# Kernel tuning notes

Hardware: AMD Instinct MI355X
Metric: run time of the kernel (lower is better)

Reference implementation:

```python
import jax, jax.numpy as jnp
import numpy as np

EPS = 1e-5

def _layernorm(x, g, b):
    # LayerNorm over last dim (head_dim), eps=1e-5 like nn.LayerNorm
    mu = jnp.mean(x, axis=-1, keepdims=True)
    var = jnp.mean(jnp.square(x - mu), axis=-1, keepdims=True)
    return (x - mu) * jax.lax.rsqrt(var + EPS) * g + b

def _rotate_half(x):
    d = x.shape[-1] // 2
    return jnp.concatenate([-x[..., d:], x[..., :d]], axis=-1)

def _apply_rotary(x, cos, sin):
    # x: [B,S,H,D]; cos/sin: [S,D] broadcast over batch and heads
    c = cos[None, :, None, :]
    s = sin[None, :, None, :]
    return x * c + _rotate_half(x) * s

def setup_inputs() -> dict:
    key = jax.random.key(0)
    ks = jax.random.split(key, 16)
    B, S, Dm = 2, 1024, 2048
    H, Hkv, Dh = 16, 4, 128
    f = lambda k, shp: (jax.random.normal(k, shp, dtype=jnp.float32) * 0.02)
    return {
        "hidden_states": jax.random.normal(ks[0], (B, S, Dm), dtype=jnp.float32),
        "cos": jax.random.uniform(ks[1], (S, Dh), dtype=jnp.float32),
        "sin": jax.random.uniform(ks[2], (S, Dh), dtype=jnp.float32),
        "Wq": f(ks[3], (H * Dh, Dm)),   "bq": jnp.zeros((H * Dh,), jnp.float32),
        "Wk": f(ks[4], (Hkv * Dh, Dm)), "bk": jnp.zeros((Hkv * Dh,), jnp.float32),
        "Wv": f(ks[5], (Hkv * Dh, Dm)), "bv": jnp.zeros((Hkv * Dh,), jnp.float32),
        "Wo": f(ks[6], (Dm, H * Dh)),   "bo": jnp.zeros((Dm,), jnp.float32),
        "qn_g": jnp.ones((Dh,), jnp.float32), "qn_b": jnp.zeros((Dh,), jnp.float32),
        "kn_g": jnp.ones((Dh,), jnp.float32), "kn_b": jnp.zeros((Dh,), jnp.float32),
        "cu_seqlens": jnp.array([0, S, 2 * S], dtype=jnp.int32),
        "max_s": 1024,
    }

def reference(hidden_states, cos, sin, Wq, bq, Wk, bk, Wv, bv, Wo, bo,
              qn_g, qn_b, kn_g, kn_b, cu_seqlens, max_s):
    B, S, Dm = hidden_states.shape
    Dh = qn_g.shape[0]
    H = Wq.shape[0] // Dh
    Hkv = Wk.shape[0] // Dh
    scale = 1.0 / jnp.sqrt(jnp.float32(Dh))

    q = (hidden_states @ Wq.T + bq).reshape(B, S, H, Dh)
    k = (hidden_states @ Wk.T + bk).reshape(B, S, Hkv, Dh)
    v = (hidden_states @ Wv.T + bv).reshape(B, S, Hkv, Dh)

    q = _apply_rotary(_layernorm(q, qn_g, qn_b), cos, sin)
    k = _apply_rotary(_layernorm(k, kn_g, kn_b), cos, sin)

    # GQA: repeat_interleave kv heads to match q heads
    n_rep = H // Hkv
    if n_rep > 1:
        k = jnp.repeat(k, n_rep, axis=2)
        v = jnp.repeat(v, n_rep, axis=2)

    # scores: [B,H,S,S]
    scores = jnp.einsum('bqhd,bkhd->bhqk', q, k) * scale
    causal = jnp.tril(jnp.ones((S, S), dtype=bool))
    scores = jnp.where(causal[None, None], scores, jnp.finfo(scores.dtype).min)
    weights = jax.nn.softmax(scores, axis=-1)
    out = jnp.einsum('bhqk,bkhd->bqhd', weights, v).reshape(B, S, H * Dh)
    return out @ Wo.T + bo
```

## Files before the change

kernel.cpp:

```cpp
#include <hip/hip_runtime.h>
#include <cmath>

typedef __attribute__((ext_vector_type(8))) short bf16x8;
typedef __attribute__((ext_vector_type(4))) short s16x4;
typedef __attribute__((ext_vector_type(4))) float f32x4;

#define MFMA_BF16 __builtin_amdgcn_mfma_f32_16x16x32_bf16

__device__ __forceinline__ float bf2f(short s) {
    unsigned u = ((unsigned)(unsigned short)s) << 16;
    return __builtin_bit_cast(float, u);
}
__device__ __forceinline__ short f2bf(float f) {
    unsigned u = __builtin_bit_cast(unsigned, f);
    u += 0x7fffu + ((u >> 16) & 1u);
    return (short)(u >> 16);
}

__device__ __forceinline__ void gl_lds16(const short* gp, short* lp) {
    __builtin_amdgcn_global_load_lds(
        (const __attribute__((address_space(1))) unsigned int*)gp,
        (__attribute__((address_space(3))) unsigned int*)lp, 16, 0, 0);
}

__global__ __launch_bounds__(256) void cvt5(
    const float* s0, short* d0, int n0,
    const float* s1, short* d1, int n1,
    const float* s2, short* d2, int n2,
    const float* s3, short* d3, int n3,
    const float* s4, short* d4, int n4)
{
    long long i = (long long)blockIdx.x * 1024 + threadIdx.x * 4;
    const float* s; short* d;
    if      (i < n0)                  { s = s0; d = d0; }
    else if ((i -= n0) < n1)          { s = s1; d = d1; }
    else if ((i -= n1) < n2)          { s = s2; d = d2; }
    else if ((i -= n2) < n3)          { s = s3; d = d3; }
    else      { i -= n3;                s = s4; d = d4; }
    float4 v = *(const float4*)(s + i);
    s16x4 o;
    o[0] = f2bf(v.x); o[1] = f2bf(v.y); o[2] = f2bf(v.z); o[3] = f2bf(v.w);
    *(s16x4*)(d + i) = o;
}

template <int MODE>
__global__ __launch_bounds__(256) void gemm_t(
    const short* __restrict__ A, const short* __restrict__ W,
    const float* __restrict__ bq, const float* __restrict__ bk,
    const float* __restrict__ bv,
    short* __restrict__ qo, short* __restrict__ ko, short* __restrict__ vo,
    float* __restrict__ fo,
    int M, int K, int S, int Hkv, int Nq, int Nkv, int N)
{
    __shared__ __align__(16) short As[2][2 * 8 * 512];
    __shared__ __align__(16) short Bs[2][2 * 4 * 512];

    const int w    = threadIdx.x >> 6;
    const int lane = threadIdx.x & 63;
    const int l15  = lane & 15;
    const int quad = lane >> 4;
    const int wy   = w >> 1;
    const int wx   = w & 1;
    const int m0   = blockIdx.y * 128;
    const int n0   = blockIdx.x * 64;

    const short* Ab = A + (size_t)m0 * K;
    const short* Wb = W + (size_t)n0 * K;

    const int srow = lane >> 2;
    const int scol = ((lane & 3) ^ ((srow >> 1) & 3)) * 8;
    auto stage = [&](int buf, int kofs) {
#pragma unroll
        for (int h2 = 0; h2 < 2; h2++) {
#pragma unroll
            for (int i = 0; i < 2; i++) {
                const int c = 2 * w + i;
                gl_lds16(Ab + (size_t)(c * 16 + srow) * K + kofs + h2 * 32 + scol,
                         As[buf] + h2 * 4096 + c * 512 + lane * 8);
            }
            gl_lds16(Wb + (size_t)(w * 16 + srow) * K + kofs + h2 * 32 + scol,
                     Bs[buf] + h2 * 2048 + w * 512 + lane * 8);
        }
    };

    f32x4 acc[4][2];
#pragma unroll
    for (int i = 0; i < 4; i++)
#pragma unroll
        for (int j = 0; j < 2; j++) acc[i][j] = f32x4{0.f, 0.f, 0.f, 0.f};

    const int ridx = (l15 * 4 + (quad ^ ((l15 >> 1) & 3))) * 8;
    const int nk = K / 64;
    stage(0, 0);
    __syncthreads();

    for (int kt = 0; kt < nk; kt++) {
        const int cur = kt & 1;
        if (kt + 1 < nk) stage(cur ^ 1, (kt + 1) * 64);

#pragma unroll
        for (int h2 = 0; h2 < 2; h2++) {
            bf16x8 af[4], bfr[2];
#pragma unroll
            for (int i = 0; i < 4; i++)
                af[i] = *(const bf16x8*)(As[cur] + h2 * 4096 + (wy * 4 + i) * 512 + ridx);
#pragma unroll
            for (int j = 0; j < 2; j++)
                bfr[j] = *(const bf16x8*)(Bs[cur] + h2 * 2048 + (wx * 2 + j) * 512 + ridx);
#pragma unroll
            for (int i = 0; i < 4; i++)
#pragma unroll
                for (int j = 0; j < 2; j++)
                    acc[i][j] = MFMA_BF16(af[i], bfr[j], acc[i][j], 0, 0, 0);
        }
        __syncthreads();
    }

#pragma unroll
    for (int i = 0; i < 4; i++) {
#pragma unroll
        for (int j = 0; j < 2; j++) {
            const int col = n0 + wx * 32 + j * 16 + l15;
#pragma unroll
            for (int r = 0; r < 4; r++) {
                const int row = m0 + wy * 64 + i * 16 + quad * 4 + r;
                float v = acc[i][j][r];
                if constexpr (MODE == 0) {
                    if (col < Nq) {
                        qo[(size_t)row * Nq + col] = f2bf(v + bq[col]);
                    } else if (col < Nq + Nkv) {
                        int cn = col - Nq;
                        ko[(size_t)row * Nkv + cn] = f2bf(v + bk[cn]);
                    } else {
                        int cn = col - Nq - Nkv;
                        int b  = row / S, s = row - b * S;
                        int hk = cn >> 7, dh = cn & 127;
                        vo[(size_t)((b * Hkv + hk) * 128 + dh) * S + s] = f2bf(v + bv[cn]);
                    }
                } else {
                    fo[(size_t)row * N + col] = v + bq[col];
                }
            }
        }
    }
}

__global__ __launch_bounds__(256) void ln_rope2(
    const short* __restrict__ Xq, short* __restrict__ Yq,
    const short* __restrict__ Xk, short* __restrict__ Yk,
    const float* __restrict__ qg, const float* __restrict__ qbe,
    const float* __restrict__ kg, const float* __restrict__ kbe,
    const float* __restrict__ cosp, const float* __restrict__ sinp,
    int H, int Hkv, int S, int nq)
{
    int gw = blockIdx.x * 4 + (threadIdx.x >> 6);
    const int lane = threadIdx.x & 63;
    const short* X; short* Y; const float* g; const float* bt; int Hc;
    if (gw < nq) { X = Xq; Y = Yq; g = qg; bt = qbe; Hc = H; }
    else { gw -= nq; X = Xk; Y = Yk; g = kg; bt = kbe; Hc = Hkv; }

    const int h  = gw % Hc;
    const int rs = gw / Hc;
    const int b  = rs / S;
    const int s  = rs - b * S;

    const short* x = X + ((size_t)rs * Hc + h) * 128;
    float x0 = bf2f(x[lane]), x1 = bf2f(x[lane + 64]);

    float sum = x0 + x1;
    float sq  = x0 * x0 + x1 * x1;
#pragma unroll
    for (int off = 32; off > 0; off >>= 1) {
        sum += __shfl_xor(sum, off, 64);
        sq  += __shfl_xor(sq, off, 64);
    }
    float mu  = sum * (1.f / 128.f);
    float var = sq * (1.f / 128.f) - mu * mu;
    float rinv = rsqrtf(var + 1e-5f);

    float y0 = (x0 - mu) * rinv * g[lane]      + bt[lane];
    float y1 = (x1 - mu) * rinv * g[lane + 64] + bt[lane + 64];

    float c0 = cosp[(size_t)s * 128 + lane];
    float c1 = cosp[(size_t)s * 128 + lane + 64];
    float s0 = sinp[(size_t)s * 128 + lane];
    float s1 = sinp[(size_t)s * 128 + lane + 64];

    float o0 = y0 * c0 - y1 * s0;
    float o1 = y1 * c1 + y0 * s1;

    short* yp = Y + ((size_t)(b * Hc + h) * S + s) * 128;
    yp[lane]      = f2bf(o0);
    yp[lane + 64] = f2bf(o1);
}

__global__ __launch_bounds__(256, 2) void attn(
    const short* __restrict__ Q, const short* __restrict__ Kt,
    const short* __restrict__ Vt, short* __restrict__ O,
    int S, int H, int Hkv, int nrep, float scale)
{
    __shared__ __align__(16) short Ks[2][16 * 512];
    __shared__ __align__(16) short Vs[2][16 * 512];
    __shared__ __align__(16) short P[4][16][72];

    const int w    = threadIdx.x >> 6;
    const int lane = threadIdx.x & 63;
    const int l15  = lane & 15;
    const int quad = lane >> 4;
    const int bh   = blockIdx.x;
    const int h    = bh % H;
    const int b    = bh / H;
    const int nyt  = gridDim.y;
    const int y    = blockIdx.y;
    const int qblk = (y < (nyt >> 1)) ? (nyt - 1 - y) : (y - (nyt >> 1));
    const int hk   = h / nrep;
    const int m0   = qblk * 64 + w * 16;
    const int qpos = m0 + l15;

    const short* qb = Q  + (size_t)(b * H + h) * S * 128;
    const short* kb = Kt + (size_t)(b * Hkv + hk) * S * 128;
    const short* vb = Vt + (size_t)(b * Hkv + hk) * 128 * S;

    auto stage = [&](int buf, int j0) {
#pragma unroll
        for (int i = 0; i < 8; i++) {
            if (w < 2) {
                const int s = w * 8 + i;
                const int t = s >> 2, c = s & 3;
                gl_lds16(kb + (size_t)(j0 + t * 16 + l15) * 128 + c * 32 + quad * 8,
                         Ks[buf] + s * 512 + lane * 8);
            } else {
                const int u = (w - 2) * 8 + i;
                const int c = u >> 1, hf = u & 1;
                gl_lds16(vb + (size_t)(c * 16 + l15) * S + j0 + hf * 32 + quad * 8,
                         Vs[buf] + u * 512 + lane * 8);
            }
        }
    };

    bf16x8 qf[4];
#pragma unroll
    for (int c = 0; c < 4; c++)
        qf[c] = *(const bf16x8*)(qb + (size_t)(m0 + l15) * 128 + c * 32 + quad * 8);

    f32x4 of[8];
#pragma unroll
    for (int c = 0; c < 8; c++) of[c] = f32x4{0.f, 0.f, 0.f, 0.f};
    float m_s = -1e30f, l_s = 0.f;
    const float c2 = scale * 1.44269504f;

    const int nkt = qblk + 1;
    stage(0, 0);
    __syncthreads();

    for (int kt = 0; kt < nkt; kt++) {
        const int cur = kt & 1;
        if (kt + 1 < nkt) stage(cur ^ 1, (kt + 1) * 64);

        const short* Kb = Ks[cur];
        const short* Vb = Vs[cur];
        const int j0 = kt * 64;

        f32x4 sc[4];
#pragma unroll
        for (int t = 0; t < 4; t++) sc[t] = f32x4{0.f, 0.f, 0.f, 0.f};
#pragma unroll
        for (int c = 0; c < 4; c++)
#pragma unroll
            for (int t = 0; t < 4; t++) {
                bf16x8 kf = *(const bf16x8*)(Kb + (t * 4 + c) * 512 + lane * 8);
                sc[t] = MFMA_BF16(kf, qf[c], sc[t], 0, 0, 0);
            }

        float v[4][4];
        float mx = -1e30f;
#pragma unroll
        for (int t = 0; t < 4; t++)
#pragma unroll
            for (int r = 0; r < 4; r++) {
                float s_ = sc[t][r];
                if (j0 + t * 16 + quad * 4 + r > qpos) s_ = -1e30f;
                v[t][r] = s_;
                mx = fmaxf(mx, s_);
            }
        mx = fmaxf(mx, __shfl_xor(mx, 16, 64));
        mx = fmaxf(mx, __shfl_xor(mx, 32, 64));
        float mnew  = fmaxf(m_s, mx);
        float mc    = mnew * c2;
        float alpha = exp2f(m_s * c2 - mc);
        float sum = 0.f;
        float p[4][4];
#pragma unroll
        for (int t = 0; t < 4; t++)
#pragma unroll
            for (int r = 0; r < 4; r++) {
                p[t][r] = exp2f(__builtin_fmaf(v[t][r], c2, -mc));
                sum += p[t][r];
            }
        sum += __shfl_xor(sum, 16, 64);
        sum += __shfl_xor(sum, 32, 64);
        l_s = l_s * alpha + sum;
        m_s = mnew;

#pragma unroll
        for (int c = 0; c < 8; c++) {
            f32x4 t = of[c];
            t[0] *= alpha; t[1] *= alpha; t[2] *= alpha; t[3] *= alpha;
            of[c] = t;
        }

#pragma unroll
        for (int t = 0; t < 4; t++) {
            s16x4 pk;
#pragma unroll
            for (int r = 0; r < 4; r++) pk[r] = f2bf(p[t][r]);
            *(s16x4*)(&P[w][l15][t * 16 + quad * 4]) = pk;
        }
        bf16x8 pb0 = *(const bf16x8*)(&P[w][l15][quad * 8]);
        bf16x8 pb1 = *(const bf16x8*)(&P[w][l15][32 + quad * 8]);

#pragma unroll
        for (int c = 0; c < 8; c++) {
            bf16x8 vf0 = *(const bf16x8*)(Vb + (c * 2 + 0) * 512 + lane * 8);
            bf16x8 vf1 = *(const bf16x8*)(Vb + (c * 2 + 1) * 512 + lane * 8);
            of[c] = MFMA_BF16(vf0, pb0, of[c], 0, 0, 0);
            of[c] = MFMA_BF16(vf1, pb1, of[c], 0, 0, 0);
        }
        __syncthreads();
    }

    const int HDh = H * 128;
    const float rinv = 1.0f / l_s;
    short* orow = O + ((size_t)b * S + qpos) * HDh + h * 128;
#pragma unroll
    for (int c = 0; c < 8; c++) {
        s16x4 ov;
#pragma unroll
        for (int r = 0; r < 4; r++) ov[r] = f2bf(of[c][r] * rinv);
        *(s16x4*)(orow + c * 16 + quad * 4) = ov;
    }
}

extern "C" void kernel_launch(void* const* d_in, const int* in_sizes, int n_in,
                              void* d_out, int out_size, void* d_ws, size_t ws_size,
                              hipStream_t stream) {
    const float* hs   = (const float*)d_in[0];
    const float* cosp = (const float*)d_in[1];
    const float* sinp = (const float*)d_in[2];
    const float* Wq   = (const float*)d_in[3];
    const float* bq   = (const float*)d_in[4];
    const float* Wk   = (const float*)d_in[5];
    const float* bk   = (const float*)d_in[6];
    const float* Wv   = (const float*)d_in[7];
    const float* bv   = (const float*)d_in[8];
    const float* Wo   = (const float*)d_in[9];
    const float* bo   = (const float*)d_in[10];
    const float* qg   = (const float*)d_in[11];
    const float* qb_  = (const float*)d_in[12];
    const float* kg   = (const float*)d_in[13];
    const float* kb_  = (const float*)d_in[14];

    const int Dh    = in_sizes[11];
    const int Dm    = in_sizes[10];
    const int HDh   = in_sizes[4];
    const int H     = HDh / Dh;
    const int HkvDh = in_sizes[6];
    const int Hkv   = HkvDh / Dh;
    const int S     = in_sizes[1] / Dh;
    const int B     = in_sizes[0] / (S * Dm);
    const int M     = B * S;
    const int nrep  = H / Hkv;

    char* ws = (char*)d_ws;
    short* hsb  = (short*)ws;  ws += (size_t)M * Dm      * 2;
    short* Wqb  = (short*)ws;  ws += (size_t)HDh * Dm    * 2;
    short* Wkb  = (short*)ws;  ws += (size_t)HkvDh * Dm  * 2;
    short* Wvb  = (short*)ws;  ws += (size_t)HkvDh * Dm  * 2;
    short* Wob  = (short*)ws;  ws += (size_t)Dm * HDh    * 2;
    short* qg16 = (short*)ws;  ws += (size_t)M * HDh     * 2;
    short* kg16 = (short*)ws;  ws += (size_t)M * HkvDh   * 2;
    short* qbuf = (short*)ws;  ws += (size_t)M * HDh     * 2;
    short* kbuf = (short*)ws;  ws += (size_t)M * HkvDh   * 2;
    short* vbuf = (short*)ws;  ws += (size_t)M * HkvDh   * 2;
    short* abuf = qg16;

    dim3 blk(256);
    const int n0 = M * Dm, n1 = HDh * Dm, n2 = HkvDh * Dm, n3 = HkvDh * Dm, n4 = Dm * HDh;
    cvt5<<<dim3((n0 + n1 + n2 + n3 + n4) / 1024), blk, 0, stream>>>(
        hs, hsb, n0, Wq, Wqb, n1, Wk, Wkb, n2, Wv, Wvb, n3, Wo, Wob, n4);

    const int Ntot = HDh + 2 * HkvDh;
    gemm_t<0><<<dim3(Ntot / 64, M / 128), blk, 0, stream>>>(
        hsb, Wqb, bq, bk, bv, qg16, kg16, vbuf, nullptr,
        M, Dm, S, Hkv, HDh, HkvDh, Ntot);

    const int nq = M * H;
    ln_rope2<<<dim3((nq + M * Hkv) / 4), blk, 0, stream>>>(
        qg16, qbuf, kg16, kbuf, qg, qb_, kg, kb_, cosp, sinp, H, Hkv, S, nq);

    const float scale = 1.0f / sqrtf((float)Dh);
    attn<<<dim3(H * B, S / 64), blk, 0, stream>>>(qbuf, kbuf, vbuf, abuf, S, H, Hkv, nrep, scale);

    gemm_t<1><<<dim3(Dm / 64, M / 128), blk, 0, stream>>>(
        abuf, Wob, bo, nullptr, nullptr, nullptr, nullptr, nullptr, (float*)d_out,
        M, HDh, S, Hkv, Dm, 0, Dm);
}
```

Before: 242.8 us.

## Deepen GEMM pipeline to four-stage ring with 32-wide K tiles

Replaces the two-buffer, 64-wide-K staging in the projection GEMM with a four-slot ring of 32-wide K tiles, keeping three tiles of global-to-LDS loads in flight. Explicit s_waitcnt vmcnt counters wait only for the tile about to be consumed, followed by a single barrier per iteration instead of a full sync after each tile. The aim is to hide global load latency better and cut barrier stalls. In exchange there are twice as many loop iterations with fewer MFMAs each, and correctness depends on the hand-counted vmcnt values staying in step with the compiler's instruction ordering.

```diff
diff --git a/kernel.cpp b/kernel.cpp
--- a/kernel.cpp
+++ b/kernel.cpp
@@ -52,8 +52,8 @@
     float* __restrict__ fo,
     int M, int K, int S, int Hkv, int Nq, int Nkv, int N)
 {
-    __shared__ __align__(16) short As[2][2 * 8 * 512];
-    __shared__ __align__(16) short Bs[2][2 * 4 * 512];
+    __shared__ __align__(16) short As[4][8 * 512];
+    __shared__ __align__(16) short Bs[4][4 * 512];
 
     const int w    = threadIdx.x >> 6;
     const int lane = threadIdx.x & 63;
@@ -71,16 +71,13 @@
     const int scol = ((lane & 3) ^ ((srow >> 1) & 3)) * 8;
     auto stage = [&](int buf, int kofs) {
 #pragma unroll
-        for (int h2 = 0; h2 < 2; h2++) {
-#pragma unroll
-            for (int i = 0; i < 2; i++) {
-                const int c = 2 * w + i;
-                gl_lds16(Ab + (size_t)(c * 16 + srow) * K + kofs + h2 * 32 + scol,
-                         As[buf] + h2 * 4096 + c * 512 + lane * 8);
-            }
-            gl_lds16(Wb + (size_t)(w * 16 + srow) * K + kofs + h2 * 32 + scol,
-                     Bs[buf] + h2 * 2048 + w * 512 + lane * 8);
-        }
+        for (int i = 0; i < 2; i++) {
+            const int c = 2 * w + i;
+            gl_lds16(Ab + (size_t)(c * 16 + srow) * K + kofs + scol,
+                     As[buf] + c * 512 + lane * 8);
+        }
+        gl_lds16(Wb + (size_t)(w * 16 + srow) * K + kofs + scol,
+                 Bs[buf] + w * 512 + lane * 8);
     };
 
     f32x4 acc[4][2];
@@ -90,30 +87,32 @@
         for (int j = 0; j < 2; j++) acc[i][j] = f32x4{0.f, 0.f, 0.f, 0.f};
 
     const int ridx = (l15 * 4 + (quad ^ ((l15 >> 1) & 3))) * 8;
-    const int nk = K / 64;
-    stage(0, 0);
-    __syncthreads();
+    const int nk = K / 32;
+
+#pragma unroll
+    for (int p = 0; p < 3; p++)
+        if (p < nk) stage(p, p * 32);
 
     for (int kt = 0; kt < nk; kt++) {
-        const int cur = kt & 1;
-        if (kt + 1 < nk) stage(cur ^ 1, (kt + 1) * 64);
-
-#pragma unroll
-        for (int h2 = 0; h2 < 2; h2++) {
-            bf16x8 af[4], bfr[2];
-#pragma unroll
-            for (int i = 0; i < 4; i++)
-                af[i] = *(const bf16x8*)(As[cur] + h2 * 4096 + (wy * 4 + i) * 512 + ridx);
+        if (kt < nk - 2)       asm volatile("s_waitcnt vmcnt(6)" ::: "memory");
+        else if (kt == nk - 2) asm volatile("s_waitcnt vmcnt(3)" ::: "memory");
+        else                   asm volatile("s_waitcnt vmcnt(0)" ::: "memory");
+        __builtin_amdgcn_s_barrier();
+        if (kt + 3 < nk) stage((kt + 3) & 3, (kt + 3) * 32);
+
+        const int cur = kt & 3;
+        bf16x8 af[4], bfr[2];
+#pragma unroll
+        for (int i = 0; i < 4; i++)
+            af[i] = *(const bf16x8*)(As[cur] + (wy * 4 + i) * 512 + ridx);
+#pragma unroll
+        for (int j = 0; j < 2; j++)
+            bfr[j] = *(const bf16x8*)(Bs[cur] + (wx * 2 + j) * 512 + ridx);
+#pragma unroll
+        for (int i = 0; i < 4; i++)
 #pragma unroll
             for (int j = 0; j < 2; j++)
-                bfr[j] = *(const bf16x8*)(Bs[cur] + h2 * 2048 + (wx * 2 + j) * 512 + ridx);
-#pragma unroll
-            for (int i = 0; i < 4; i++)
-#pragma unroll
-                for (int j = 0; j < 2; j++)
-                    acc[i][j] = MFMA_BF16(af[i], bfr[j], acc[i][j], 0, 0, 0);
-        }
-        __syncthreads();
+                acc[i][j] = MFMA_BF16(af[i], bfr[j], acc[i][j], 0, 0, 0);
     }
 
 #pragma unroll
```

New measurement: 261.4 us. 1.08x slower.

## Load attention K/V directly to registers and remap blocks across XCDs

Applied to the files above, without the earlier changes.

The attention kernel drops its double-buffered LDS staging of K and V tiles and the per-iteration block barrier. Each wave now loads its K and V fragments straight from global memory into registers, relying on L2/cache reuse across the four waves. Both the GEMM and attention kernels also remap block indices so that neighbouring tiles (same rows/heads) land on the same XCD, to improve L2 locality on the multi-die GPU. The cost is that each wave re-reads K/V from global memory (4x redundant traffic per block), register pressure goes up, and the launch bound no longer requests two blocks per CU.

```diff
diff --git a/kernel.cpp b/kernel.cpp
--- a/kernel.cpp
+++ b/kernel.cpp
@@ -61,8 +61,18 @@
     const int quad = lane >> 4;
     const int wy   = w >> 1;
     const int wx   = w & 1;
-    const int m0   = blockIdx.y * 128;
-    const int n0   = blockIdx.x * 64;
+
+    unsigned gx = gridDim.x, gy = gridDim.y;
+    unsigned bx = blockIdx.x, by = blockIdx.y;
+    if ((gx & 3) == 0 && (gy & 1) == 0) {
+        unsigned lin = by * gx + bx;
+        unsigned xcd = lin & 7, idx = lin >> 3;
+        unsigned n   = gx >> 2;
+        bx = (xcd & 3) * n + idx % n;
+        by = (xcd >> 2) * (gy >> 1) + idx / n;
+    }
+    const int m0 = by * 128;
+    const int n0 = bx * 64;
 
     const short* Ab = A + (size_t)m0 * K;
     const short* Wb = W + (size_t)n0 * K;
@@ -194,24 +204,31 @@
     yp[lane + 64] = f2bf(o1);
 }
 
-__global__ __launch_bounds__(256, 2) void attn(
+__global__ __launch_bounds__(256) void attn(
     const short* __restrict__ Q, const short* __restrict__ Kt,
     const short* __restrict__ Vt, short* __restrict__ O,
     int S, int H, int Hkv, int nrep, float scale)
 {
-    __shared__ __align__(16) short Ks[2][16 * 512];
-    __shared__ __align__(16) short Vs[2][16 * 512];
     __shared__ __align__(16) short P[4][16][72];
 
     const int w    = threadIdx.x >> 6;
     const int lane = threadIdx.x & 63;
     const int l15  = lane & 15;
     const int quad = lane >> 4;
-    const int bh   = blockIdx.x;
+
+    const int gx  = gridDim.x;
+    const int nyt = gridDim.y;
+    int bh, y;
+    if ((gx & 7) == 0) {
+        unsigned lin = blockIdx.y * gx + blockIdx.x;
+        unsigned xcd = lin & 7, idx = lin >> 3;
+        unsigned nx  = gx >> 3;
+        bh = xcd * nx + idx % nx;
+        y  = idx / nx;
+    } else { bh = blockIdx.x; y = blockIdx.y; }
+
     const int h    = bh % H;
     const int b    = bh / H;
-    const int nyt  = gridDim.y;
-    const int y    = blockIdx.y;
     const int qblk = (y < (nyt >> 1)) ? (nyt - 1 - y) : (y - (nyt >> 1));
     const int hk   = h / nrep;
     const int m0   = qblk * 64 + w * 16;
@@ -221,23 +238,6 @@
     const short* kb = Kt + (size_t)(b * Hkv + hk) * S * 128;
     const short* vb = Vt + (size_t)(b * Hkv + hk) * 128 * S;
 
-    auto stage = [&](int buf, int j0) {
-#pragma unroll
-        for (int i = 0; i < 8; i++) {
-            if (w < 2) {
-                const int s = w * 8 + i;
-                const int t = s >> 2, c = s & 3;
-                gl_lds16(kb + (size_t)(j0 + t * 16 + l15) * 128 + c * 32 + quad * 8,
-                         Ks[buf] + s * 512 + lane * 8);
-            } else {
-                const int u = (w - 2) * 8 + i;
-                const int c = u >> 1, hf = u & 1;
-                gl_lds16(vb + (size_t)(c * 16 + l15) * S + j0 + hf * 32 + quad * 8,
-                         Vs[buf] + u * 512 + lane * 8);
-            }
-        }
-    };
-
     bf16x8 qf[4];
 #pragma unroll
     for (int c = 0; c < 4; c++)
@@ -250,27 +250,25 @@
     const float c2 = scale * 1.44269504f;
 
     const int nkt = qblk + 1;
-    stage(0, 0);
-    __syncthreads();
-
     for (int kt = 0; kt < nkt; kt++) {
-        const int cur = kt & 1;
-        if (kt + 1 < nkt) stage(cur ^ 1, (kt + 1) * 64);
-
-        const short* Kb = Ks[cur];
-        const short* Vb = Vs[cur];
         const int j0 = kt * 64;
 
+        bf16x8 kf[16];
+#pragma unroll
+        for (int t = 0; t < 4; t++)
+#pragma unroll
+            for (int c = 0; c < 4; c++)
+                kf[t * 4 + c] = *(const bf16x8*)(
+                    kb + (size_t)(j0 + t * 16 + l15) * 128 + c * 32 + quad * 8);
+
         f32x4 sc[4];
 #pragma unroll
         for (int t = 0; t < 4; t++) sc[t] = f32x4{0.f, 0.f, 0.f, 0.f};
 #pragma unroll
         for (int c = 0; c < 4; c++)
 #pragma unroll
-            for (int t = 0; t < 4; t++) {
-                bf16x8 kf = *(const bf16x8*)(Kb + (t * 4 + c) * 512 + lane * 8);
-                sc[t] = MFMA_BF16(kf, qf[c], sc[t], 0, 0, 0);
-            }
+            for (int t = 0; t < 4; t++)
+                sc[t] = MFMA_BF16(kf[t * 4 + c], qf[c], sc[t], 0, 0, 0);
 
         float v[4][4];
         float mx = -1e30f;
@@ -288,6 +286,14 @@
         float mnew  = fmaxf(m_s, mx);
         float mc    = mnew * c2;
         float alpha = exp2f(m_s * c2 - mc);
+
+        bf16x8 vf[16];
+#pragma unroll
+        for (int c = 0; c < 8; c++) {
+            vf[c * 2 + 0] = *(const bf16x8*)(vb + (size_t)(c * 16 + l15) * S + j0 + quad * 8);
+            vf[c * 2 + 1] = *(const bf16x8*)(vb + (size_t)(c * 16 + l15) * S + j0 + 32 + quad * 8);
+        }
+
         float sum = 0.f;
         float p[4][4];
 #pragma unroll
@@ -321,12 +327,9 @@
 
 #pragma unroll
         for (int c = 0; c < 8; c++) {
-            bf16x8 vf0 = *(const bf16x8*)(Vb + (c * 2 + 0) * 512 + lane * 8);
-            bf16x8 vf1 = *(const bf16x8*)(Vb + (c * 2 + 1) * 512 + lane * 8);
-            of[c] = MFMA_BF16(vf0, pb0, of[c], 0, 0, 0);
-            of[c] = MFMA_BF16(vf1, pb1, of[c], 0, 0, 0);
-        }
-        __syncthreads();
+            of[c] = MFMA_BF16(vf[c * 2 + 0], pb0, of[c], 0, 0, 0);
+            of[c] = MFMA_BF16(vf[c * 2 + 1], pb1, of[c], 0, 0, 0);
+        }
     }
 
     const int HDh = H * 128;
```

After: 294.5 us. 1.21x slower.

## Fuse fp32-to-bf16 conversion into GEMM tile loads and remap blocks across XCDs

Applied to the files above, without the earlier changes.

Removes the separate conversion kernel that cast hidden states and all weight matrices to bf16. The GEMMs now load fp32 tiles through registers, convert them, and write bf16 into LDS, with the global loads for the next tile issued before the current tile's MFMAs. This drops a launch and a full read-write pass over the weights and activations. In exchange the GEMMs read twice as many bytes per tile, re-read the fp32 weights once per M-block, and use more registers. A block-index swizzle is also added so that neighbouring tiles land on the same XCD, which should improve L2 reuse.

```diff
diff --git a/kernel.cpp b/kernel.cpp
--- a/kernel.cpp
+++ b/kernel.cpp
@@ -23,29 +23,11 @@
         (__attribute__((address_space(3))) unsigned int*)lp, 16, 0, 0);
 }
 
-__global__ __launch_bounds__(256) void cvt5(
-    const float* s0, short* d0, int n0,
-    const float* s1, short* d1, int n1,
-    const float* s2, short* d2, int n2,
-    const float* s3, short* d3, int n3,
-    const float* s4, short* d4, int n4)
-{
-    long long i = (long long)blockIdx.x * 1024 + threadIdx.x * 4;
-    const float* s; short* d;
-    if      (i < n0)                  { s = s0; d = d0; }
-    else if ((i -= n0) < n1)          { s = s1; d = d1; }
-    else if ((i -= n1) < n2)          { s = s2; d = d2; }
-    else if ((i -= n2) < n3)          { s = s3; d = d3; }
-    else      { i -= n3;                s = s4; d = d4; }
-    float4 v = *(const float4*)(s + i);
-    s16x4 o;
-    o[0] = f2bf(v.x); o[1] = f2bf(v.y); o[2] = f2bf(v.z); o[3] = f2bf(v.w);
-    *(s16x4*)(d + i) = o;
-}
-
 template <int MODE>
 __global__ __launch_bounds__(256) void gemm_t(
-    const short* __restrict__ A, const short* __restrict__ W,
+    const float* __restrict__ Af, const short* __restrict__ Abf,
+    const float* __restrict__ Wqf, const float* __restrict__ Wkf,
+    const float* __restrict__ Wvf,
     const float* __restrict__ bq, const float* __restrict__ bk,
     const float* __restrict__ bv,
     short* __restrict__ qo, short* __restrict__ ko, short* __restrict__ vo,
@@ -61,26 +43,82 @@
     const int quad = lane >> 4;
     const int wy   = w >> 1;
     const int wx   = w & 1;
-    const int m0   = blockIdx.y * 128;
-    const int n0   = blockIdx.x * 64;
-
-    const short* Ab = A + (size_t)m0 * K;
-    const short* Wb = W + (size_t)n0 * K;
+
+    unsigned gx = gridDim.x, gy = gridDim.y;
+    unsigned bx = blockIdx.x, by = blockIdx.y;
+    if ((gx & 3) == 0 && (gy & 1) == 0) {
+        unsigned lin = by * gx + bx;
+        unsigned xcd = lin & 7, idx = lin >> 3;
+        unsigned n   = gx >> 2;
+        bx = (xcd & 3) * n + idx % n;
+        by = (xcd >> 2) * (gy >> 1) + idx / n;
+    }
+    const int m0 = by * 128;
+    const int n0 = bx * 64;
+
+    const float* Wb;
+    if (MODE == 1 || n0 < Nq)  Wb = Wqf + (size_t)n0 * K;
+    else if (n0 < Nq + Nkv)    Wb = Wkf + (size_t)(n0 - Nq) * K;
+    else                       Wb = Wvf + (size_t)(n0 - Nq - Nkv) * K;
+
+    const float* Abase_f = (MODE == 0) ? Af  + (size_t)m0 * K : nullptr;
+    const short* Abase_h = (MODE == 1) ? Abf + (size_t)m0 * K : nullptr;
 
     const int srow = lane >> 2;
     const int scol = ((lane & 3) ^ ((srow >> 1) & 3)) * 8;
-    auto stage = [&](int buf, int kofs) {
+
+    float4 ra[2][2][2];
+    float4 rb[2][2];
+
+    auto loadW = [&](int kofs) {
 #pragma unroll
         for (int h2 = 0; h2 < 2; h2++) {
+            const float* p = Wb + (size_t)(w * 16 + srow) * K + kofs + h2 * 32 + scol;
+            rb[h2][0] = *(const float4*)p;
+            rb[h2][1] = *(const float4*)(p + 4);
+        }
+    };
+    auto loadA = [&](int kofs) {
+#pragma unroll
+        for (int h2 = 0; h2 < 2; h2++)
 #pragma unroll
             for (int i = 0; i < 2; i++) {
                 const int c = 2 * w + i;
-                gl_lds16(Ab + (size_t)(c * 16 + srow) * K + kofs + h2 * 32 + scol,
+                const float* p = Abase_f + (size_t)(c * 16 + srow) * K + kofs + h2 * 32 + scol;
+                ra[h2][i][0] = *(const float4*)p;
+                ra[h2][i][1] = *(const float4*)(p + 4);
+            }
+    };
+    auto stageA_lds = [&](int buf, int kofs) {
+#pragma unroll
+        for (int h2 = 0; h2 < 2; h2++)
+#pragma unroll
+            for (int i = 0; i < 2; i++) {
+                const int c = 2 * w + i;
+                gl_lds16(Abase_h + (size_t)(c * 16 + srow) * K + kofs + h2 * 32 + scol,
                          As[buf] + h2 * 4096 + c * 512 + lane * 8);
             }
-            gl_lds16(Wb + (size_t)(w * 16 + srow) * K + kofs + h2 * 32 + scol,
-                     Bs[buf] + h2 * 2048 + w * 512 + lane * 8);
-        }
+    };
+    auto cvt8 = [&](float4 lo, float4 hi) {
+        bf16x8 v;
+        v[0] = f2bf(lo.x); v[1] = f2bf(lo.y); v[2] = f2bf(lo.z); v[3] = f2bf(lo.w);
+        v[4] = f2bf(hi.x); v[5] = f2bf(hi.y); v[6] = f2bf(hi.z); v[7] = f2bf(hi.w);
+        return v;
+    };
+    auto writeW = [&](int buf) {
+#pragma unroll
+        for (int h2 = 0; h2 < 2; h2++)
+            *(bf16x8*)(Bs[buf] + h2 * 2048 + w * 512 + lane * 8) = cvt8(rb[h2][0], rb[h2][1]);
+    };
+    auto writeA = [&](int buf) {
+#pragma unroll
+        for (int h2 = 0; h2 < 2; h2++)
+#pragma unroll
+            for (int i = 0; i < 2; i++) {
+                const int c = 2 * w + i;
+                *(bf16x8*)(As[buf] + h2 * 4096 + c * 512 + lane * 8) =
+                    cvt8(ra[h2][i][0], ra[h2][i][1]);
+            }
     };
 
     f32x4 acc[4][2];
@@ -91,12 +129,22 @@
 
     const int ridx = (l15 * 4 + (quad ^ ((l15 >> 1) & 3))) * 8;
     const int nk = K / 64;
-    stage(0, 0);
+
+    if constexpr (MODE == 0) { loadA(0); } else { stageA_lds(0, 0); }
+    loadW(0);
+    if constexpr (MODE == 0) writeA(0);
+    writeW(0);
     __syncthreads();
 
     for (int kt = 0; kt < nk; kt++) {
         const int cur = kt & 1;
-        if (kt + 1 < nk) stage(cur ^ 1, (kt + 1) * 64);
+        const int nxt = cur ^ 1;
+        const bool pf = (kt + 1 < nk);
+        if (pf) {
+            if constexpr (MODE == 0) loadA((kt + 1) * 64);
+            else                     stageA_lds(nxt, (kt + 1) * 64);
+            loadW((kt + 1) * 64);
+        }
 
 #pragma unroll
         for (int h2 = 0; h2 < 2; h2++) {
@@ -112,6 +160,11 @@
 #pragma unroll
                 for (int j = 0; j < 2; j++)
                     acc[i][j] = MFMA_BF16(af[i], bfr[j], acc[i][j], 0, 0, 0);
+        }
+
+        if (pf) {
+            if constexpr (MODE == 0) writeA(nxt);
+            writeW(nxt);
         }
         __syncthreads();
     }
@@ -372,11 +425,6 @@
     const int nrep  = H / Hkv;
 
     char* ws = (char*)d_ws;
-    short* hsb  = (short*)ws;  ws += (size_t)M * Dm      * 2;
-    short* Wqb  = (short*)ws;  ws += (size_t)HDh * Dm    * 2;
-    short* Wkb  = (short*)ws;  ws += (size_t)HkvDh * Dm  * 2;
-    short* Wvb  = (short*)ws;  ws += (size_t)HkvDh * Dm  * 2;
-    short* Wob  = (short*)ws;  ws += (size_t)Dm * HDh    * 2;
     short* qg16 = (short*)ws;  ws += (size_t)M * HDh     * 2;
     short* kg16 = (short*)ws;  ws += (size_t)M * HkvDh   * 2;
     short* qbuf = (short*)ws;  ws += (size_t)M * HDh     * 2;
@@ -385,13 +433,10 @@
     short* abuf = qg16;
 
     dim3 blk(256);
-    const int n0 = M * Dm, n1 = HDh * Dm, n2 = HkvDh * Dm, n3 = HkvDh * Dm, n4 = Dm * HDh;
-    cvt5<<<dim3((n0 + n1 + n2 + n3 + n4) / 1024), blk, 0, stream>>>(
-        hs, hsb, n0, Wq, Wqb, n1, Wk, Wkb, n2, Wv, Wvb, n3, Wo, Wob, n4);
-
     const int Ntot = HDh + 2 * HkvDh;
     gemm_t<0><<<dim3(Ntot / 64, M / 128), blk, 0, stream>>>(
-        hsb, Wqb, bq, bk, bv, qg16, kg16, vbuf, nullptr,
+        hs, nullptr, Wq, Wk, Wv, bq, bk, bv,
+        qg16, kg16, vbuf, nullptr,
         M, Dm, S, Hkv, HDh, HkvDh, Ntot);
 
     const int nq = M * H;
@@ -402,6 +447,7 @@
     attn<<<dim3(H * B, S / 64), blk, 0, stream>>>(qbuf, kbuf, vbuf, abuf, S, H, Hkv, nrep, scale);
 
     gemm_t<1><<<dim3(Dm / 64, M / 128), blk, 0, stream>>>(
-        abuf, Wob, bo, nullptr, nullptr, nullptr, nullptr, nullptr, (float*)d_out,
+        nullptr, abuf, Wo, nullptr, nullptr, bo, nullptr, nullptr,
+        nullptr, nullptr, nullptr, (float*)d_out,
         M, HDh, S, Hkv, Dm, 0, Dm);
 }
```

New measurement: 270.4 us. 11.4% more time.
